# Optimization experiments

Measured on AMD Instinct MI355X. Metric: run time of the kernel, lower is better.

## Reference

```python
import jax, jax.numpy as jnp
import numpy as np

L, T, B, D, H, DFF = 6, 128, 256, 512, 8, 2048
SUB = D // H  # 64


def setup_inputs() -> dict:
    key = jax.random.key(0)
    ks = iter(jax.random.split(key, 16))

    def w(shape, fan):
        return jax.random.normal(next(ks), shape, jnp.float32) * (1.0 / np.sqrt(fan))

    return dict(
        src=jax.random.normal(next(ks), (T, B, D), jnp.float32),
        srcc=jax.random.normal(next(ks), (T, B, D), jnp.float32),
        spatio_w=w((L, D, D), D), spatio_b=jnp.zeros((L, D), jnp.float32),
        temporal_w=w((L, D, D), D), temporal_b=jnp.zeros((L, D), jnp.float32),
        attn_w=w((L, H, 2 * SUB), 2 * SUB), attn_b=jnp.zeros((L, H), jnp.float32),
        msg_w=w((L, H, SUB, SUB), SUB), msg_b=jnp.zeros((L, H, SUB), jnp.float32),
        agg_w=w((L, D, D), D), agg_b=jnp.zeros((L, D), jnp.float32),
        lin1_w=w((L, DFF, D), D), lin1_b=jnp.zeros((L, DFF), jnp.float32),
        lin2_w=w((L, D, DFF), DFF), lin2_b=jnp.zeros((L, D), jnp.float32),
        ln1_g=jnp.ones((L, D), jnp.float32), ln1_b=jnp.zeros((L, D), jnp.float32),
        ln2_g=jnp.ones((L, D), jnp.float32), ln2_b=jnp.zeros((L, D), jnp.float32),
    )


def _layernorm(x, g, b):
    m = jnp.mean(x, -1, keepdims=True)
    v = jnp.mean(jnp.square(x - m), -1, keepdims=True)
    return (x - m) * jax.lax.rsqrt(v + 1e-5) * g + b


def _layer(src, srcc, p):
    # src, srcc: [T, B, D]
    s = jax.nn.relu(jnp.einsum('tbd,ed->tbe', srcc, p['sw']) + p['sb'])
    t = jax.nn.relu(jnp.einsum('tbd,ed->tbe', src, p['tw']) + p['tb'])
    s_r = s.reshape(T, B, H, SUB).transpose(2, 1, 0, 3)  # [H, B, T, sub]
    t_r = t.reshape(T, B, H, SUB).transpose(2, 1, 0, 3)
    feat = jnp.concatenate([s_r, t_r], axis=-1)          # [H, B, T, 2*sub]
    # Per-head scoring Linear(2*sub -> 1), batched over heads
    scores = jnp.einsum('hbtc,hc->hbt', feat, p['aw']) + p['ab'][:, None, None]
    # Source applies softmax over dim=0 of the per-head [B, T, 1] tensor -> batch axis
    wts = jax.nn.softmax(scores, axis=1)[..., None]       # [H, B, T, 1]
    # Per-head message Linear(sub -> sub) on elementwise product
    msg = jnp.einsum('hbts,hus->hbtu', s_r * t_r, p['mw']) + p['mb'][:, None, None, :]
    wm = (wts * msg).transpose(1, 2, 0, 3).reshape(B, T, D)  # concat heads -> [B, T, D]
    agg = jnp.einsum('btd,ed->bte', jax.nn.relu(wm), p['gw']) + p['gb']
    x = _layernorm(src.transpose(1, 0, 2) + agg, p['n1g'], p['n1b'])
    h1 = jax.nn.relu(jnp.einsum('btd,fd->btf', x, p['w1']) + p['b1'])
    y = jnp.einsum('btf,df->btd', h1, p['w2']) + p['b2']
    x = _layernorm(x + y, p['n2g'], p['n2b'])
    return x.transpose(1, 0, 2)  # back to [T, B, D]


def reference(src, srcc, spatio_w, spatio_b, temporal_w, temporal_b, attn_w, attn_b,
              msg_w, msg_b, agg_w, agg_b, lin1_w, lin1_b, lin2_w, lin2_b,
              ln1_g, ln1_b, ln2_g, ln2_b):
    out = src
    for i in range(L):
        p = dict(sw=spatio_w[i], sb=spatio_b[i], tw=temporal_w[i], tb=temporal_b[i],
                 aw=attn_w[i], ab=attn_b[i], mw=msg_w[i], mb=msg_b[i],
                 gw=agg_w[i], gb=agg_b[i], w1=lin1_w[i], b1=lin1_b[i],
                 w2=lin2_w[i], b2=lin2_b[i], n1g=ln1_g[i], n1b=ln1_b[i],
                 n2g=ln2_g[i], n2b=ln2_b[i])
        out = _layer(out, srcc, p)
    return out
```

## Files before the change

kernel.cpp:

```cpp
#include <hip/hip_runtime.h>
#include <hip/hip_bf16.h>
#include <stdint.h>

constexpr int cL = 6, cT = 128, cB = 256, cD = 512, cH = 8, cF = 2048, cS = 64;
constexpr int cM = cT * cB;

typedef __bf16 bf16_t;
typedef __bf16 bf16x8 __attribute__((ext_vector_type(8)));
typedef __bf16 bf16x4 __attribute__((ext_vector_type(4)));
typedef float f32x4 __attribute__((ext_vector_type(4)));

__global__ __launch_bounds__(256) void cast_kernel(const float* __restrict__ in,
                                                   bf16_t* __restrict__ out, int n) {
  int i = (blockIdx.x * 256 + threadIdx.x) * 4;
  if (i >= n) return;
  float4 v = *(const float4*)(in + i);
  bf16x4 o;
  o[0] = (bf16_t)v.x; o[1] = (bf16_t)v.y; o[2] = (bf16_t)v.z; o[3] = (bf16_t)v.w;
  *(bf16x4*)(out + i) = o;
}

__global__ __launch_bounds__(256) void gemm_bt_kernel(
    const bf16_t* __restrict__ A0, const bf16_t* __restrict__ Bw0,
    const float* __restrict__ bias0, bf16_t* __restrict__ C0,
    const bf16_t* __restrict__ A1, const bf16_t* __restrict__ Bw1,
    const float* __restrict__ bias1, bf16_t* __restrict__ C1,
    int K, int N, int relu) {
  __shared__ __align__(16) bf16_t lds[4 * 128 * 64];
  bf16_t* const As0 = lds;
  bf16_t* const Bs0 = lds + 8192;
  bf16_t* const As1 = lds + 16384;
  bf16_t* const Bs1 = lds + 24576;
  const int tid = threadIdx.x;
  const bf16_t* A  = (blockIdx.z == 0) ? A0 : A1;
  const bf16_t* Bw = (blockIdx.z == 0) ? Bw0 : Bw1;
  const float* bias = (blockIdx.z == 0) ? bias0 : bias1;
  bf16_t* C = (blockIdx.z == 0) ? C0 : C1;
  int bx, by;
  {
    const unsigned gx = gridDim.x;
    const unsigned d = blockIdx.x + gx * blockIdx.y;
    const unsigned nwg = gx * gridDim.y;
    unsigned w = d;
    if ((nwg & 7u) == 0u) w = (d & 7u) * (nwg >> 3) + (d >> 3);
    bx = (int)(w % gx);
    by = (int)(w / gx);
  }
  const size_t m0 = (size_t)by * 128;
  const size_t n0 = (size_t)bx * 128;
  const int lane = tid & 63;
  const int wv = tid >> 6;
  const int wm = (wv >> 1) * 64;
  const int wn = (wv & 1) * 64;
  const int srow = tid >> 3;
  const int sslot = tid & 7;
  const int ssw = sslot ^ (srow & 7);
  const bf16_t* gA = A + (m0 + srow) * K + ssw * 8;
  const bf16_t* gB = Bw + (n0 + srow) * K + ssw * 8;
  f32x4 acc[4][4];
  const f32x4 zero = {0.f, 0.f, 0.f, 0.f};
#pragma unroll
  for (int i = 0; i < 4; i++)
#pragma unroll
    for (int j = 0; j < 4; j++) acc[i][j] = zero;
  const int fr = lane & 15;
  const int kq = (lane >> 4) * 8;
  const int swr = fr & 7;

  auto stage = [&](bf16_t* Ad, bf16_t* Bd, int k0) {
#pragma unroll
    for (int i = 0; i < 4; i++)
      __builtin_amdgcn_global_load_lds(
          (__attribute__((address_space(1))) void*)(gA + (size_t)i * 32 * K + k0),
          (__attribute__((address_space(3))) void*)(Ad + i * 2048 + tid * 8), 16, 0, 0);
#pragma unroll
    for (int i = 0; i < 4; i++)
      __builtin_amdgcn_global_load_lds(
          (__attribute__((address_space(1))) void*)(gB + (size_t)i * 32 * K + k0),
          (__attribute__((address_space(3))) void*)(Bd + i * 2048 + tid * 8), 16, 0, 0);
  };
  auto compute = [&](const bf16_t* As_, const bf16_t* Bs_) {
#pragma unroll
    for (int kk = 0; kk < 2; kk++) {
      const int ls = kk * 4 + (kq >> 3);
      const int sc = (ls ^ swr) * 8;
      bf16x8 af[4], bfr[4];
#pragma unroll
      for (int i = 0; i < 4; i++)
        af[i] = *(const bf16x8*)(As_ + (wm + i * 16 + fr) * 64 + sc);
#pragma unroll
      for (int j = 0; j < 4; j++)
        bfr[j] = *(const bf16x8*)(Bs_ + (wn + j * 16 + fr) * 64 + sc);
#pragma unroll
      for (int i = 0; i < 4; i++)
#pragma unroll
        for (int j = 0; j < 4; j++)
          acc[i][j] = __builtin_amdgcn_mfma_f32_16x16x32_bf16(af[i], bfr[j], acc[i][j], 0, 0, 0);
    }
  };

  const int nt = K >> 6;
  bf16_t *ca = As0, *cb = Bs0, *na = As1, *nb = Bs1;
  stage(ca, cb, 0);
  int pk = 64;
  for (int t = 0; t < nt; ++t) {
    if (t + 1 < nt) {
      stage(na, nb, pk);
      pk += 64;
      asm volatile("s_waitcnt vmcnt(8)" ::: "memory");
    } else {
      asm volatile("s_waitcnt vmcnt(0)" ::: "memory");
    }
    __builtin_amdgcn_s_barrier();
    __builtin_amdgcn_sched_barrier(0);
    compute(ca, cb);
    __builtin_amdgcn_s_barrier();
    __builtin_amdgcn_sched_barrier(0);
    bf16_t* t0 = ca; ca = na; na = t0;
    bf16_t* t1 = cb; cb = nb; nb = t1;
  }

  constexpr int CP = 136;
  bf16_t* const ct = lds;
  const int row0 = wm + (lane >> 4) * 4;
#pragma unroll
  for (int j = 0; j < 4; j++) {
    const int col = wn + j * 16 + fr;
    const float bv = bias[n0 + col];
#pragma unroll
    for (int i = 0; i < 4; i++) {
#pragma unroll
      for (int r = 0; r < 4; r++) {
        float v = acc[i][j][r] + bv;
        if (relu) v = fmaxf(v, 0.f);
        ct[(row0 + i * 16 + r) * CP + col] = (bf16_t)v;
      }
    }
  }
  __syncthreads();
  const int erc = (tid & 15) * 8;
  const int err = tid >> 4;
#pragma unroll
  for (int p = 0; p < 8; p++) {
    const int row = p * 16 + err;
    bf16x8 vv = *(const bf16x8*)(ct + row * CP + erc);
    *(bf16x8*)(C + (m0 + row) * (size_t)N + n0 + erc) = vv;
  }
}

__global__ __launch_bounds__(256) void attn_kernel(
    const bf16_t* __restrict__ s, const bf16_t* __restrict__ t,
    const float* __restrict__ aw, const float* __restrict__ ab,
    const float* __restrict__ mw, const float* __restrict__ mb,
    bf16_t* __restrict__ wm) {
  constexpr int P = cS + 8;
  __shared__ __align__(16) bf16_t p[cB][P];
  __shared__ __align__(16) bf16_t w[cS][P];
  __shared__ float score[cB];
  __shared__ float wt[cB];
  __shared__ float red[8];
  const int h = blockIdx.x;
  const int tt = blockIdx.y;
  const int tid = threadIdx.x;
  const int lane = tid & 63;
  const int wv = tid >> 6;
  {
    const int u = tid >> 2;
    const int c16 = (tid & 3) * 16;
    const float* wr = mw + ((size_t)h * cS + u) * cS + c16;
#pragma unroll
    for (int q = 0; q < 2; q++) {
      float4 a = *(const float4*)(wr + q * 8);
      float4 bq = *(const float4*)(wr + q * 8 + 4);
      bf16x8 o;
      o[0] = (bf16_t)a.x; o[1] = (bf16_t)a.y; o[2] = (bf16_t)a.z; o[3] = (bf16_t)a.w;
      o[4] = (bf16_t)bq.x; o[5] = (bf16_t)bq.y; o[6] = (bf16_t)bq.z; o[7] = (bf16_t)bq.w;
      *(bf16x8*)(&w[u][c16 + q * 8]) = o;
    }
  }
  const int col8 = (tid & 7) * 8;
  const float* aws = aw + (size_t)h * 2 * cS;
  const float* awt = aws + cS;
#pragma unroll
  for (int r8 = 0; r8 < 8; r8++) {
    const int row = (tid >> 3) + r8 * 32;
    const size_t g = ((size_t)tt * cB + row) * cD + h * cS + col8;
    bf16x8 sv = *(const bf16x8*)(s + g);
    bf16x8 tv = *(const bf16x8*)(t + g);
    bf16x8 pv;
    float sc = 0.f;
#pragma unroll
    for (int i = 0; i < 8; i++) {
      float sf = (float)sv[i], tf = (float)tv[i];
      pv[i] = (bf16_t)(sf * tf);
      sc += sf * aws[col8 + i] + tf * awt[col8 + i];
    }
    *(bf16x8*)(&p[row][col8]) = pv;
    sc += __shfl_xor(sc, 1);
    sc += __shfl_xor(sc, 2);
    sc += __shfl_xor(sc, 4);
    if ((tid & 7) == 0) score[row] = sc;
  }
  __syncthreads();
  {
    float v = score[tid];
    float m = v;
#pragma unroll
    for (int o = 32; o; o >>= 1) m = fmaxf(m, __shfl_xor(m, o));
    if (lane == 0) red[wv] = m;
    __syncthreads();
    const float mx = fmaxf(fmaxf(red[0], red[1]), fmaxf(red[2], red[3]));
    const float e = __expf(v - mx);
    float sm = e;
#pragma unroll
    for (int o = 32; o; o >>= 1) sm += __shfl_xor(sm, o);
    if (lane == 0) red[4 + wv] = sm;
    __syncthreads();
    const float tot = red[4] + red[5] + red[6] + red[7];
    wt[tid] = e / tot;
  }
  __syncthreads();
  const int rbase = wv * 64;
  const int fr = lane & 15;
  const int kq = (lane >> 4) * 8;
  f32x4 acc[4][4];
  const f32x4 zero = {0.f, 0.f, 0.f, 0.f};
#pragma unroll
  for (int i = 0; i < 4; i++)
#pragma unroll
    for (int j = 0; j < 4; j++) acc[i][j] = zero;
#pragma unroll
  for (int k0 = 0; k0 < cS; k0 += 32) {
    bf16x8 af[4], bfr[4];
#pragma unroll
    for (int i = 0; i < 4; i++)
      af[i] = *(const bf16x8*)(&p[rbase + i * 16 + fr][k0 + kq]);
#pragma unroll
    for (int j = 0; j < 4; j++)
      bfr[j] = *(const bf16x8*)(&w[j * 16 + fr][k0 + kq]);
#pragma unroll
    for (int i = 0; i < 4; i++)
#pragma unroll
      for (int j = 0; j < 4; j++)
        acc[i][j] = __builtin_amdgcn_mfma_f32_16x16x32_bf16(af[i], bfr[j], acc[i][j], 0, 0, 0);
  }
  const int row0 = (lane >> 4) * 4;
#pragma unroll
  for (int j = 0; j < 4; j++) {
    const int col = j * 16 + fr;
    const float mbv = mb[h * cS + col];
#pragma unroll
    for (int i = 0; i < 4; i++) {
#pragma unroll
      for (int r = 0; r < 4; r++) {
        const int brow = rbase + i * 16 + row0 + r;
        float v = (acc[i][j][r] + mbv) * wt[brow];
        v = fmaxf(v, 0.f);
        wm[((size_t)tt * cB + brow) * cD + h * cS + col] = (bf16_t)v;
      }
    }
  }
}

__global__ __launch_bounds__(64) void ln_kernel(
    const float* __restrict__ inaF, const bf16_t* __restrict__ inaB, int a_tmajor,
    const float* __restrict__ inbF, const bf16_t* __restrict__ inbB, int b_tmajor,
    const float* __restrict__ gam, const float* __restrict__ bet,
    float* __restrict__ outF, int oF_tmajor, bf16_t* __restrict__ outB, int oB_tmajor,
    int rid0) {
  const int local = blockIdx.x;
  const int rid = rid0 + local;
  const int b = rid >> 7;
  const int t = rid & (cT - 1);
  const size_t tmaj = ((size_t)t * cB + b) * cD;
  const size_t bmaj = (size_t)rid * cD;
  const int d0 = threadIdx.x * 8;
  float v[8];
  if (inbB) {
    bf16x8 a = *(const bf16x8*)(inbB + (b_tmajor ? tmaj : bmaj) + d0);
#pragma unroll
    for (int i = 0; i < 8; i++) v[i] = (float)a[i];
  } else {
    const float4* pb = (const float4*)(inbF + (size_t)local * cD + d0);
    float4 b0 = pb[0], b1 = pb[1];
    v[0] = b0.x; v[1] = b0.y; v[2] = b0.z; v[3] = b0.w;
    v[4] = b1.x; v[5] = b1.y; v[6] = b1.z; v[7] = b1.w;
  }
  const size_t aoff = (a_tmajor ? tmaj : bmaj) + d0;
  if (inaF) {
    const float4* pa = (const float4*)(inaF + aoff);
    float4 a0 = pa[0], a1 = pa[1];
    v[0] += a0.x; v[1] += a0.y; v[2] += a0.z; v[3] += a0.w;
    v[4] += a1.x; v[5] += a1.y; v[6] += a1.z; v[7] += a1.w;
  } else {
    bf16x8 a = *(const bf16x8*)(inaB + aoff);
#pragma unroll
    for (int i = 0; i < 8; i++) v[i] += (float)a[i];
  }
  float sm = 0.f, sq = 0.f;
#pragma unroll
  for (int i = 0; i < 8; i++) { sm += v[i]; sq += v[i] * v[i]; }
#pragma unroll
  for (int o = 32; o; o >>= 1) { sm += __shfl_xor(sm, o); sq += __shfl_xor(sq, o); }
  const float mean = sm * (1.f / cD);
  const float var = sq * (1.f / cD) - mean * mean;
  const float rs = rsqrtf(var + 1e-5f);
  const float4 g0 = *(const float4*)(gam + d0);
  const float4 g1 = *(const float4*)(gam + d0 + 4);
  const float4 e0 = *(const float4*)(bet + d0);
  const float4 e1 = *(const float4*)(bet + d0 + 4);
  float o8[8];
  o8[0] = (v[0] - mean) * rs * g0.x + e0.x;
  o8[1] = (v[1] - mean) * rs * g0.y + e0.y;
  o8[2] = (v[2] - mean) * rs * g0.z + e0.z;
  o8[3] = (v[3] - mean) * rs * g0.w + e0.w;
  o8[4] = (v[4] - mean) * rs * g1.x + e1.x;
  o8[5] = (v[5] - mean) * rs * g1.y + e1.y;
  o8[6] = (v[6] - mean) * rs * g1.z + e1.z;
  o8[7] = (v[7] - mean) * rs * g1.w + e1.w;
  if (outF) {
    const size_t ooff = (oF_tmajor ? tmaj : bmaj) + d0;
    *(float4*)(outF + ooff) = make_float4(o8[0], o8[1], o8[2], o8[3]);
    *(float4*)(outF + ooff + 4) = make_float4(o8[4], o8[5], o8[6], o8[7]);
  }
  if (outB) {
    bf16x8 ob;
#pragma unroll
    for (int i = 0; i < 8; i++) ob[i] = (bf16_t)o8[i];
    *(bf16x8*)(outB + (oB_tmajor ? tmaj : bmaj) + d0) = ob;
  }
}

extern "C" void kernel_launch(void* const* d_in, const int* in_sizes, int n_in,
                              void* d_out, int out_size, void* d_ws, size_t ws_size,
                              hipStream_t stream) {
  (void)in_sizes; (void)n_in; (void)out_size;
  const float* src        = (const float*)d_in[0];
  const float* srcc       = (const float*)d_in[1];
  const float* spatio_w   = (const float*)d_in[2];
  const float* spatio_b   = (const float*)d_in[3];
  const float* temporal_w = (const float*)d_in[4];
  const float* temporal_b = (const float*)d_in[5];
  const float* attn_w     = (const float*)d_in[6];
  const float* attn_b     = (const float*)d_in[7];
  const float* msg_w      = (const float*)d_in[8];
  const float* msg_b      = (const float*)d_in[9];
  const float* agg_w      = (const float*)d_in[10];
  const float* agg_b      = (const float*)d_in[11];
  const float* lin1_w     = (const float*)d_in[12];
  const float* lin1_b     = (const float*)d_in[13];
  const float* lin2_w     = (const float*)d_in[14];
  const float* lin2_b     = (const float*)d_in[15];
  const float* ln1_g      = (const float*)d_in[16];
  const float* ln1_bb     = (const float*)d_in[17];
  const float* ln2_g      = (const float*)d_in[18];
  const float* ln2_bb     = (const float*)d_in[19];

  size_t off = 0;
  auto alloc = [&](size_t nbytes) -> void* {
    void* p = (char*)d_ws + off;
    off += (nbytes + 255) & ~(size_t)255;
    return p;
  };
  const size_t nTok = (size_t)cM;
  const size_t actB = nTok * cD * sizeof(bf16_t);

  bf16_t* sw_bf   = (bf16_t*)alloc((size_t)cL * cD * cD * 2);
  bf16_t* tw_bf   = (bf16_t*)alloc((size_t)cL * cD * cD * 2);
  bf16_t* gw_bf   = (bf16_t*)alloc((size_t)cL * cD * cD * 2);
  bf16_t* w1_bf   = (bf16_t*)alloc((size_t)cL * cF * cD * 2);
  bf16_t* w2_bf   = (bf16_t*)alloc((size_t)cL * cD * cF * 2);
  bf16_t* srcc_bf = (bf16_t*)alloc(actB);
  bf16_t* cur_bf  = (bf16_t*)alloc(actB);
  bf16_t* s_bf    = (bf16_t*)alloc(actB);
  bf16_t* t_bf    = (bf16_t*)alloc(actB);
  bf16_t* wmx_bf  = (bf16_t*)alloc(actB);
  const size_t fixed_end = off;

  const size_t residBytes = nTok * cD * 4;
  const size_t slack = 1 << 20;
  size_t avail = (ws_size > fixed_end + slack) ? (ws_size - fixed_end - slack) : 0;
  auto sBytes = [&](int Mc) {
    size_t h1 = (size_t)Mc * cF * 2;
    return h1 > actB ? h1 : actB;
  };
  bool useResid; int Mc;
  if      (avail >= residBytes + sBytes(cM))    { useResid = true;  Mc = cM; }
  else if (avail >= residBytes + sBytes(16384)) { useResid = true;  Mc = 16384; }
  else if (avail >= sBytes(cM))                 { useResid = false; Mc = cM; }
  else if (avail >= sBytes(16384))              { useResid = false; Mc = 16384; }
  else                                          { useResid = false; Mc = 8192; }
  float*  resid = useResid ? (float*)alloc(residBytes) : nullptr;
  void*   S     = alloc(sBytes(Mc));
  bf16_t* aggB  = (bf16_t*)S;
  bf16_t* h1_bf = (bf16_t*)S;
  const int nCh = cM / Mc;

  auto cast = [&](const float* i, bf16_t* o, size_t n) {
    cast_kernel<<<dim3((unsigned)((n / 4 + 255) / 256)), dim3(256), 0, stream>>>(i, o, (int)n);
  };
  cast(spatio_w, sw_bf, (size_t)cL * cD * cD);
  cast(temporal_w, tw_bf, (size_t)cL * cD * cD);
  cast(agg_w, gw_bf, (size_t)cL * cD * cD);
  cast(lin1_w, w1_bf, (size_t)cL * cF * cD);
  cast(lin2_w, w2_bf, (size_t)cL * cD * cF);
  cast(srcc, srcc_bf, nTok * cD);
  cast(src, cur_bf, nTok * cD);

  const dim3 blk(256);
  for (int l = 0; l < cL; l++) {
    const bf16_t* swl = sw_bf + (size_t)l * cD * cD;
    const bf16_t* twl = tw_bf + (size_t)l * cD * cD;
    const bf16_t* gwl = gw_bf + (size_t)l * cD * cD;
    const bf16_t* w1l = w1_bf + (size_t)l * cF * cD;
    const bf16_t* w2l = w2_bf + (size_t)l * cD * cF;

    gemm_bt_kernel<<<dim3(4, cM / 128, 2), blk, 0, stream>>>(
        srcc_bf, swl, spatio_b + l * cD, s_bf,
        cur_bf, twl, temporal_b + l * cD, t_bf, cD, cD, 1);
    attn_kernel<<<dim3(cH, cT), blk, 0, stream>>>(
        s_bf, t_bf, attn_w + (size_t)l * cH * 2 * cS, attn_b + l * cH,
        msg_w + (size_t)l * cH * cS * cS, msg_b + l * cH * cS, wmx_bf);
    gemm_bt_kernel<<<dim3(4, cM / 128, 1), blk, 0, stream>>>(
        wmx_bf, gwl, agg_b + l * cD, aggB,
        nullptr, nullptr, nullptr, nullptr, cD, cD, 0);
    {
      const float* iaF = nullptr; const bf16_t* iaB = nullptr; int a_t = 0;
      if (useResid) { if (l == 0) { iaF = src; a_t = 1; } else { iaF = resid; } }
      else          { iaB = cur_bf; a_t = 1; }
      ln_kernel<<<dim3(cM), dim3(64), 0, stream>>>(
          iaF, iaB, a_t, nullptr, aggB, 1, ln1_g + l * cD, ln1_bb + l * cD,
          resid, 0, s_bf, 0, 0);
    }
    for (int c = 0; c < nCh; c++) {
      const int r0 = c * Mc;
      gemm_bt_kernel<<<dim3(cF / 128, Mc / 128, 1), blk, 0, stream>>>(
          s_bf + (size_t)r0 * cD, w1l, lin1_b + l * cF, h1_bf,
          nullptr, nullptr, nullptr, nullptr, cD, cF, 1);
      gemm_bt_kernel<<<dim3(4, Mc / 128, 1), blk, 0, stream>>>(
          h1_bf, w2l, lin2_b + l * cD, t_bf + (size_t)r0 * cD,
          nullptr, nullptr, nullptr, nullptr, cF, cD, 0);
    }
    {
      const float* iaF = useResid ? resid : nullptr;
      const bf16_t* iaB = useResid ? nullptr : s_bf;
      float* oF; int oFt;
      if (l == cL - 1) { oF = (float*)d_out; oFt = 1; }
      else if (useResid) { oF = resid; oFt = 0; }
      else { oF = nullptr; oFt = 0; }
      ln_kernel<<<dim3(cM), dim3(64), 0, stream>>>(
          iaF, iaB, 0, nullptr, t_bf, 0, ln2_g + l * cD, ln2_bb + l * cD,
          oF, oFt, (l == cL - 1) ? nullptr : cur_bf, 1, 0);
    }
  }
}
```

Before: 2.219 ms.

## Enlarge GEMM tiles to 256x256 with 8 waves and interleaved prefetch

```diff
diff --git a/kernel.cpp b/kernel.cpp
--- a/kernel.cpp
+++ b/kernel.cpp
@@ -20,20 +20,16 @@
   *(bf16x4*)(out + i) = o;
 }
 
-__global__ __launch_bounds__(256) void gemm_bt_kernel(
+__global__ __launch_bounds__(512, 2) void gemm_bt_kernel(
     const bf16_t* __restrict__ A0, const bf16_t* __restrict__ Bw0,
     const float* __restrict__ bias0, bf16_t* __restrict__ C0,
     const bf16_t* __restrict__ A1, const bf16_t* __restrict__ Bw1,
     const float* __restrict__ bias1, bf16_t* __restrict__ C1,
     int K, int N, int relu) {
-  __shared__ __align__(16) bf16_t lds[4 * 128 * 64];
-  bf16_t* const As0 = lds;
-  bf16_t* const Bs0 = lds + 8192;
-  bf16_t* const As1 = lds + 16384;
-  bf16_t* const Bs1 = lds + 24576;
+  __shared__ __align__(16) bf16_t lds[65536];
   const int tid = threadIdx.x;
-  const bf16_t* A  = (blockIdx.z == 0) ? A0 : A1;
-  const bf16_t* Bw = (blockIdx.z == 0) ? Bw0 : Bw1;
+  const bf16_t* A   = (blockIdx.z == 0) ? A0 : A1;
+  const bf16_t* Bw  = (blockIdx.z == 0) ? Bw0 : Bw1;
   const float* bias = (blockIdx.z == 0) ? bias0 : bias1;
   bf16_t* C = (blockIdx.z == 0) ? C0 : C1;
   int bx, by;
@@ -46,105 +42,123 @@
     bx = (int)(w % gx);
     by = (int)(w / gx);
   }
-  const size_t m0 = (size_t)by * 128;
-  const size_t n0 = (size_t)bx * 128;
+  const size_t m0 = (size_t)by * 256;
+  const size_t n0 = (size_t)bx * 256;
   const int lane = tid & 63;
   const int wv = tid >> 6;
-  const int wm = (wv >> 1) * 64;
-  const int wn = (wv & 1) * 64;
+  const int wm = (wv >> 2) * 128;
+  const int wn = (wv & 3) * 64;
+  const int fr = lane & 15;
+  const int fr7 = fr & 7;
+  const int kq4 = lane >> 4;
+  const int ck0 = ((kq4 ^ fr7) * 8);
+  const int ck1 = (((kq4 + 4) ^ fr7) * 8);
   const int srow = tid >> 3;
-  const int sslot = tid & 7;
-  const int ssw = sslot ^ (srow & 7);
+  const int ssw = (tid & 7) ^ (srow & 7);
   const bf16_t* gA = A + (m0 + srow) * K + ssw * 8;
   const bf16_t* gB = Bw + (n0 + srow) * K + ssw * 8;
-  f32x4 acc[4][4];
-  const f32x4 zero = {0.f, 0.f, 0.f, 0.f};
-#pragma unroll
-  for (int i = 0; i < 4; i++)
-#pragma unroll
-    for (int j = 0; j < 4; j++) acc[i][j] = zero;
-  const int fr = lane & 15;
-  const int kq = (lane >> 4) * 8;
-  const int swr = fr & 7;
-
-  auto stage = [&](bf16_t* Ad, bf16_t* Bd, int k0) {
+
+  auto stage = [&](int buf, int k0) {
+    bf16_t* Ad = lds + buf * 32768;
+    bf16_t* Bd = Ad + 16384;
 #pragma unroll
     for (int i = 0; i < 4; i++)
       __builtin_amdgcn_global_load_lds(
-          (__attribute__((address_space(1))) void*)(gA + (size_t)i * 32 * K + k0),
-          (__attribute__((address_space(3))) void*)(Ad + i * 2048 + tid * 8), 16, 0, 0);
+          (__attribute__((address_space(1))) void*)(gA + (size_t)(i * 64) * K + k0),
+          (__attribute__((address_space(3))) void*)(Ad + i * 4096 + tid * 8), 16, 0, 0);
 #pragma unroll
     for (int i = 0; i < 4; i++)
       __builtin_amdgcn_global_load_lds(
-          (__attribute__((address_space(1))) void*)(gB + (size_t)i * 32 * K + k0),
-          (__attribute__((address_space(3))) void*)(Bd + i * 2048 + tid * 8), 16, 0, 0);
+          (__attribute__((address_space(1))) void*)(gB + (size_t)(i * 64) * K + k0),
+          (__attribute__((address_space(3))) void*)(Bd + i * 4096 + tid * 8), 16, 0, 0);
   };
-  auto compute = [&](const bf16_t* As_, const bf16_t* Bs_) {
-#pragma unroll
-    for (int kk = 0; kk < 2; kk++) {
-      const int ls = kk * 4 + (kq >> 3);
-      const int sc = (ls ^ swr) * 8;
-      bf16x8 af[4], bfr[4];
-#pragma unroll
-      for (int i = 0; i < 4; i++)
-        af[i] = *(const bf16x8*)(As_ + (wm + i * 16 + fr) * 64 + sc);
-#pragma unroll
-      for (int j = 0; j < 4; j++)
-        bfr[j] = *(const bf16x8*)(Bs_ + (wn + j * 16 + fr) * 64 + sc);
-#pragma unroll
-      for (int i = 0; i < 4; i++)
-#pragma unroll
-        for (int j = 0; j < 4; j++)
-          acc[i][j] = __builtin_amdgcn_mfma_f32_16x16x32_bf16(af[i], bfr[j], acc[i][j], 0, 0, 0);
-    }
-  };
+
+  f32x4 acc[8][4];
+  const f32x4 zero = {0.f, 0.f, 0.f, 0.f};
+#pragma unroll
+  for (int i = 0; i < 8; i++)
+#pragma unroll
+    for (int j = 0; j < 4; j++) acc[i][j] = zero;
 
   const int nt = K >> 6;
-  bf16_t *ca = As0, *cb = Bs0, *na = As1, *nb = Bs1;
-  stage(ca, cb, 0);
-  int pk = 64;
+  int cur = 0;
+  stage(0, 0);
+  asm volatile("s_waitcnt vmcnt(0)" ::: "memory");
+  __builtin_amdgcn_s_barrier();
+  __builtin_amdgcn_sched_barrier(0);
   for (int t = 0; t < nt; ++t) {
-    if (t + 1 < nt) {
-      stage(na, nb, pk);
-      pk += 64;
-      asm volatile("s_waitcnt vmcnt(8)" ::: "memory");
-    } else {
-      asm volatile("s_waitcnt vmcnt(0)" ::: "memory");
-    }
-    __builtin_amdgcn_s_barrier();
-    __builtin_amdgcn_sched_barrier(0);
-    compute(ca, cb);
-    __builtin_amdgcn_s_barrier();
-    __builtin_amdgcn_sched_barrier(0);
-    bf16_t* t0 = ca; ca = na; na = t0;
-    bf16_t* t1 = cb; cb = nb; nb = t1;
-  }
-
-  constexpr int CP = 136;
-  bf16_t* const ct = lds;
-  const int row0 = wm + (lane >> 4) * 4;
-#pragma unroll
-  for (int j = 0; j < 4; j++) {
-    const int col = wn + j * 16 + fr;
-    const float bv = bias[n0 + col];
-#pragma unroll
-    for (int i = 0; i < 4; i++) {
-#pragma unroll
-      for (int r = 0; r < 4; r++) {
-        float v = acc[i][j][r] + bv;
-        if (relu) v = fmaxf(v, 0.f);
-        ct[(row0 + i * 16 + r) * CP + col] = (bf16_t)v;
+    const bf16_t* pA = lds + cur * 32768;
+    const bf16_t* pB = pA + 16384;
+    bf16x8 bfr[4][2];
+#pragma unroll
+    for (int q = 0; q < 4; q++) {
+      if (q == 0) {
+        if (t + 1 < nt) stage(cur ^ 1, (t + 1) * 64);
+#pragma unroll
+        for (int nf = 0; nf < 4; nf++) {
+          const int rb = (wn + nf * 16 + fr) * 64;
+          bfr[nf][0] = *(const bf16x8*)(pB + rb + ck0);
+          bfr[nf][1] = *(const bf16x8*)(pB + rb + ck1);
+        }
       }
-    }
-  }
-  __syncthreads();
-  const int erc = (tid & 15) * 8;
-  const int err = tid >> 4;
-#pragma unroll
-  for (int p = 0; p < 8; p++) {
-    const int row = p * 16 + err;
-    bf16x8 vv = *(const bf16x8*)(ct + row * CP + erc);
-    *(bf16x8*)(C + (m0 + row) * (size_t)N + n0 + erc) = vv;
+      bf16x8 af[2][2];
+#pragma unroll
+      for (int i = 0; i < 2; i++) {
+        const int ra = (wm + (q * 2 + i) * 16 + fr) * 64;
+        af[i][0] = *(const bf16x8*)(pA + ra + ck0);
+        af[i][1] = *(const bf16x8*)(pA + ra + ck1);
+      }
+      __builtin_amdgcn_sched_barrier(0);
+      __builtin_amdgcn_s_barrier();
+      __builtin_amdgcn_s_setprio(1);
+#pragma unroll
+      for (int i = 0; i < 2; i++)
+#pragma unroll
+        for (int nf = 0; nf < 4; nf++) {
+          acc[q * 2 + i][nf] = __builtin_amdgcn_mfma_f32_16x16x32_bf16(
+              af[i][0], bfr[nf][0], acc[q * 2 + i][nf], 0, 0, 0);
+          acc[q * 2 + i][nf] = __builtin_amdgcn_mfma_f32_16x16x32_bf16(
+              af[i][1], bfr[nf][1], acc[q * 2 + i][nf], 0, 0, 0);
+        }
+      __builtin_amdgcn_s_setprio(0);
+      __builtin_amdgcn_sched_barrier(0);
+      if (q == 3 && t + 1 < nt)
+        asm volatile("s_waitcnt vmcnt(0)" ::: "memory");
+      __builtin_amdgcn_s_barrier();
+      __builtin_amdgcn_sched_barrier(0);
+    }
+    cur ^= 1;
+  }
+
+  constexpr int CP = 264;
+  const int wr = wv >> 2;
+  const int row0 = (lane >> 4) * 4;
+  for (int p = 0; p < 2; ++p) {
+    if (p) __syncthreads();
+    if (wr == p) {
+#pragma unroll
+      for (int nf = 0; nf < 4; nf++) {
+        const int c = wn + nf * 16 + fr;
+        const float bv = bias[n0 + c];
+#pragma unroll
+        for (int mf = 0; mf < 8; mf++)
+#pragma unroll
+          for (int r = 0; r < 4; r++) {
+            float v = acc[mf][nf][r] + bv;
+            if (relu) v = fmaxf(v, 0.f);
+            lds[(mf * 16 + row0 + r) * CP + c] = (bf16_t)v;
+          }
+      }
+    }
+    __syncthreads();
+#pragma unroll
+    for (int u8 = 0; u8 < 8; u8++) {
+      const int u = u8 * 512 + tid;
+      const int row = u >> 5;
+      const int col = (u & 31) * 8;
+      bf16x8 vv = *(const bf16x8*)(lds + row * CP + col);
+      *(bf16x8*)(C + (m0 + p * 128 + row) * (size_t)N + n0 + col) = vv;
+    }
   }
 }
 
@@ -407,7 +421,7 @@
   cast(srcc, srcc_bf, nTok * cD);
   cast(src, cur_bf, nTok * cD);
 
-  const dim3 blk(256);
+  const dim3 blk(512);
   for (int l = 0; l < cL; l++) {
     const bf16_t* swl = sw_bf + (size_t)l * cD * cD;
     const bf16_t* twl = tw_bf + (size_t)l * cD * cD;
@@ -415,13 +429,13 @@
     const bf16_t* w1l = w1_bf + (size_t)l * cF * cD;
     const bf16_t* w2l = w2_bf + (size_t)l * cD * cF;
 
-    gemm_bt_kernel<<<dim3(4, cM / 128, 2), blk, 0, stream>>>(
+    gemm_bt_kernel<<<dim3(cD / 256, cM / 256, 2), blk, 0, stream>>>(
         srcc_bf, swl, spatio_b + l * cD, s_bf,
         cur_bf, twl, temporal_b + l * cD, t_bf, cD, cD, 1);
-    attn_kernel<<<dim3(cH, cT), blk, 0, stream>>>(
+    attn_kernel<<<dim3(cH, cT), dim3(256), 0, stream>>>(
         s_bf, t_bf, attn_w + (size_t)l * cH * 2 * cS, attn_b + l * cH,
         msg_w + (size_t)l * cH * cS * cS, msg_b + l * cH * cS, wmx_bf);
-    gemm_bt_kernel<<<dim3(4, cM / 128, 1), blk, 0, stream>>>(
+    gemm_bt_kernel<<<dim3(cD / 256, cM / 256, 1), blk, 0, stream>>>(
         wmx_bf, gwl, agg_b + l * cD, aggB,
         nullptr, nullptr, nullptr, nullptr, cD, cD, 0);
     {
@@ -434,10 +448,10 @@
     }
     for (int c = 0; c < nCh; c++) {
       const int r0 = c * Mc;
-      gemm_bt_kernel<<<dim3(cF / 128, Mc / 128, 1), blk, 0, stream>>>(
+      gemm_bt_kernel<<<dim3(cF / 256, Mc / 256, 1), blk, 0, stream>>>(
           s_bf + (size_t)r0 * cD, w1l, lin1_b + l * cF, h1_bf,
           nullptr, nullptr, nullptr, nullptr, cD, cF, 1);
-      gemm_bt_kernel<<<dim3(4, Mc / 128, 1), blk, 0, stream>>>(
+      gemm_bt_kernel<<<dim3(cD / 256, Mc / 256, 1), blk, 0, stream>>>(
           h1_bf, w2l, lin2_b + l * cD, t_bf + (size_t)r0 * cD,
           nullptr, nullptr, nullptr, nullptr, cF, cD, 0);
     }
```

New measurement: 3.112 ms. 1.4x slower.
